# Kernel tuning notes

Measured on AMD Instinct MI355X. Metric: run time of the kernel, lower is better.

Reference implementation:

```python
import jax, jax.numpy as jnp
import numpy as np

CODEBOOK_SIZE = 1024
EMBED_DIM = 64
COMMITMENT_COST = 0.25


def setup_inputs() -> dict:
    key = jax.random.key(0)
    k1, k2 = jax.random.split(key)
    z = jax.random.normal(k1, (8, EMBED_DIM, 8192), dtype=jnp.float32)
    # torch init: uniform(-1/codebook_size, 1/codebook_size)
    codebook_weight = jax.random.uniform(
        k2, (CODEBOOK_SIZE, EMBED_DIM), dtype=jnp.float32,
        minval=-1.0 / CODEBOOK_SIZE, maxval=1.0 / CODEBOOK_SIZE)
    return {"z": z, "codebook_weight": codebook_weight}


def reference(z, codebook_weight):
    B, D, T = z.shape
    # [B*T, D]
    z_flat = jnp.transpose(z, (0, 2, 1)).reshape(-1, D)
    # squared euclidean distances to each code: ||z||^2 - 2 z.W^T + ||W||^2
    distances = (jnp.sum(z_flat * z_flat, axis=1, keepdims=True)
                 - 2.0 * z_flat @ codebook_weight.T
                 + jnp.sum(codebook_weight * codebook_weight, axis=1))
    codes = jnp.argmin(distances, axis=1)  # [B*T]
    z_q = codebook_weight[codes].reshape(B, T, D).transpose(0, 2, 1)  # [B, D, T]
    commitment_loss = jnp.mean((jax.lax.stop_gradient(z_q) - z) ** 2)
    codebook_loss = jnp.mean((z_q - jax.lax.stop_gradient(z)) ** 2)
    vq_loss = codebook_loss + COMMITMENT_COST * commitment_loss
    # straight-through estimator
    z_q_st = z + jax.lax.stop_gradient(z_q - z)
    return z_q_st, vq_loss, codes
```

## Files before the change

### kernel.cpp

```cpp
#include <hip/hip_runtime.h>


#define T_DIM 8192
#define D_DIM 64
#define C_DIM 1024
#define B_DIM 8
#define NROWS (B_DIM * T_DIM)
#define NELEM (B_DIM * D_DIM * T_DIM)
#define SEGS 4
#define CODES_PER_SEG (C_DIM / SEGS)
#define EPI_BLOCKS (NELEM / 4 / 256)

#define R64(M) M(0) M(1) M(2) M(3) M(4) M(5) M(6) M(7) \
  M(8) M(9) M(10) M(11) M(12) M(13) M(14) M(15) \
  M(16) M(17) M(18) M(19) M(20) M(21) M(22) M(23) \
  M(24) M(25) M(26) M(27) M(28) M(29) M(30) M(31) \
  M(32) M(33) M(34) M(35) M(36) M(37) M(38) M(39) \
  M(40) M(41) M(42) M(43) M(44) M(45) M(46) M(47) \
  M(48) M(49) M(50) M(51) M(52) M(53) M(54) M(55) \
  M(56) M(57) M(58) M(59) M(60) M(61) M(62) M(63)

#define SQ_(x) __fmul_rn(x, x)
#define AD_(a, b) __fadd_rn(a, b)

#define PAIRWISE64(p, dst) \
  float pr0 = SQ_(p##0);  pr0 = AD_(pr0, SQ_(p##8));  pr0 = AD_(pr0, SQ_(p##16)); pr0 = AD_(pr0, SQ_(p##24)); pr0 = AD_(pr0, SQ_(p##32)); pr0 = AD_(pr0, SQ_(p##40)); pr0 = AD_(pr0, SQ_(p##48)); pr0 = AD_(pr0, SQ_(p##56)); \
  float pr1 = SQ_(p##1);  pr1 = AD_(pr1, SQ_(p##9));  pr1 = AD_(pr1, SQ_(p##17)); pr1 = AD_(pr1, SQ_(p##25)); pr1 = AD_(pr1, SQ_(p##33)); pr1 = AD_(pr1, SQ_(p##41)); pr1 = AD_(pr1, SQ_(p##49)); pr1 = AD_(pr1, SQ_(p##57)); \
  float pr2 = SQ_(p##2);  pr2 = AD_(pr2, SQ_(p##10)); pr2 = AD_(pr2, SQ_(p##18)); pr2 = AD_(pr2, SQ_(p##26)); pr2 = AD_(pr2, SQ_(p##34)); pr2 = AD_(pr2, SQ_(p##42)); pr2 = AD_(pr2, SQ_(p##50)); pr2 = AD_(pr2, SQ_(p##58)); \
  float pr3 = SQ_(p##3);  pr3 = AD_(pr3, SQ_(p##11)); pr3 = AD_(pr3, SQ_(p##19)); pr3 = AD_(pr3, SQ_(p##27)); pr3 = AD_(pr3, SQ_(p##35)); pr3 = AD_(pr3, SQ_(p##43)); pr3 = AD_(pr3, SQ_(p##51)); pr3 = AD_(pr3, SQ_(p##59)); \
  float pr4 = SQ_(p##4);  pr4 = AD_(pr4, SQ_(p##12)); pr4 = AD_(pr4, SQ_(p##20)); pr4 = AD_(pr4, SQ_(p##28)); pr4 = AD_(pr4, SQ_(p##36)); pr4 = AD_(pr4, SQ_(p##44)); pr4 = AD_(pr4, SQ_(p##52)); pr4 = AD_(pr4, SQ_(p##60)); \
  float pr5 = SQ_(p##5);  pr5 = AD_(pr5, SQ_(p##13)); pr5 = AD_(pr5, SQ_(p##21)); pr5 = AD_(pr5, SQ_(p##29)); pr5 = AD_(pr5, SQ_(p##37)); pr5 = AD_(pr5, SQ_(p##45)); pr5 = AD_(pr5, SQ_(p##53)); pr5 = AD_(pr5, SQ_(p##61)); \
  float pr6 = SQ_(p##6);  pr6 = AD_(pr6, SQ_(p##14)); pr6 = AD_(pr6, SQ_(p##22)); pr6 = AD_(pr6, SQ_(p##30)); pr6 = AD_(pr6, SQ_(p##38)); pr6 = AD_(pr6, SQ_(p##46)); pr6 = AD_(pr6, SQ_(p##54)); pr6 = AD_(pr6, SQ_(p##62)); \
  float pr7 = SQ_(p##7);  pr7 = AD_(pr7, SQ_(p##15)); pr7 = AD_(pr7, SQ_(p##23)); pr7 = AD_(pr7, SQ_(p##31)); pr7 = AD_(pr7, SQ_(p##39)); pr7 = AD_(pr7, SQ_(p##47)); pr7 = AD_(pr7, SQ_(p##55)); pr7 = AD_(pr7, SQ_(p##63)); \
  float dst = AD_(AD_(AD_(pr0, pr1), AD_(pr2, pr3)), AD_(AD_(pr4, pr5), AD_(pr6, pr7)));

__global__ __launch_bounds__(256, 2)
void vq_dist_kernel(const float* __restrict__ z,
                    const float* __restrict__ cb,
                    float2* __restrict__ pairs) {
    const int tid = threadIdx.x;
    const int row = blockIdx.x * 256 + tid;
    const int seg = blockIdx.y;
    const int c0 = seg * CODES_PER_SEG;
    const int b = row >> 13;
    const int t = row & (T_DIM - 1);

    __shared__ float wsqs[CODES_PER_SEG];
    __shared__ float4 zl[16][256];

    {
        const float* wp = cb + ((size_t)(c0 + tid) << 6);
#define LOADW(k) float w##k = wp[k];
        R64(LOADW)
#undef LOADW
        PAIRWISE64(w, s)
        wsqs[tid] = s;
    }

    const float* zp = z + (size_t)b * (D_DIM * T_DIM) + t;
#define LOADZ(k) float z##k = zp[(size_t)k * T_DIM];
    R64(LOADZ)
#undef LOADZ
    PAIRWISE64(z, zsq)
    zl[ 0][tid] = make_float4(z0,  z1,  z2,  z3);
    zl[ 1][tid] = make_float4(z4,  z5,  z6,  z7);
    zl[ 2][tid] = make_float4(z8,  z9,  z10, z11);
    zl[ 3][tid] = make_float4(z12, z13, z14, z15);
    zl[ 4][tid] = make_float4(z16, z17, z18, z19);
    zl[ 5][tid] = make_float4(z20, z21, z22, z23);
    zl[ 6][tid] = make_float4(z24, z25, z26, z27);
    zl[ 7][tid] = make_float4(z28, z29, z30, z31);
    zl[ 8][tid] = make_float4(z32, z33, z34, z35);
    zl[ 9][tid] = make_float4(z36, z37, z38, z39);
    zl[10][tid] = make_float4(z40, z41, z42, z43);
    zl[11][tid] = make_float4(z44, z45, z46, z47);
    zl[12][tid] = make_float4(z48, z49, z50, z51);
    zl[13][tid] = make_float4(z52, z53, z54, z55);
    zl[14][tid] = make_float4(z56, z57, z58, z59);
    zl[15][tid] = make_float4(z60, z61, z62, z63);
    __syncthreads();

    float bestd = 3.4e38f;
    int besti = 0;
#pragma unroll 1
    for (int cc = 0; cc < CODES_PER_SEG; cc += 8) {
        const float* wp = cb + ((size_t)(c0 + cc) << 6);
        float a0 = 0.f, a1 = 0.f, a2 = 0.f, a3 = 0.f;
        float a4 = 0.f, a5 = 0.f, a6 = 0.f, a7 = 0.f;
#pragma unroll
        for (int kk = 0; kk < 16; ++kk) {
            const float4 zk = zl[kk][tid];
            const int k4 = kk << 2;
#define CHAIN(n) \
            a##n = fmaf(zk.x, wp[(n << 6) + k4 + 0], a##n); \
            a##n = fmaf(zk.y, wp[(n << 6) + k4 + 1], a##n); \
            a##n = fmaf(zk.z, wp[(n << 6) + k4 + 2], a##n); \
            a##n = fmaf(zk.w, wp[(n << 6) + k4 + 3], a##n);
            CHAIN(0) CHAIN(1) CHAIN(2) CHAIN(3)
            CHAIN(4) CHAIN(5) CHAIN(6) CHAIN(7)
#undef CHAIN
        }
        const float4 wqA = *(const float4*)(&wsqs[cc]);
        const float4 wqB = *(const float4*)(&wsqs[cc + 4]);
        float d0 = __fadd_rn(__fsub_rn(zsq, __fmul_rn(2.0f, a0)), wqA.x);
        float d1 = __fadd_rn(__fsub_rn(zsq, __fmul_rn(2.0f, a1)), wqA.y);
        float d2 = __fadd_rn(__fsub_rn(zsq, __fmul_rn(2.0f, a2)), wqA.z);
        float d3 = __fadd_rn(__fsub_rn(zsq, __fmul_rn(2.0f, a3)), wqA.w);
        float d4 = __fadd_rn(__fsub_rn(zsq, __fmul_rn(2.0f, a4)), wqB.x);
        float d5 = __fadd_rn(__fsub_rn(zsq, __fmul_rn(2.0f, a5)), wqB.y);
        float d6 = __fadd_rn(__fsub_rn(zsq, __fmul_rn(2.0f, a6)), wqB.z);
        float d7 = __fadd_rn(__fsub_rn(zsq, __fmul_rn(2.0f, a7)), wqB.w);
        if (d0 < bestd) { bestd = d0; besti = c0 + cc + 0; }
        if (d1 < bestd) { bestd = d1; besti = c0 + cc + 1; }
        if (d2 < bestd) { bestd = d2; besti = c0 + cc + 2; }
        if (d3 < bestd) { bestd = d3; besti = c0 + cc + 3; }
        if (d4 < bestd) { bestd = d4; besti = c0 + cc + 4; }
        if (d5 < bestd) { bestd = d5; besti = c0 + cc + 5; }
        if (d6 < bestd) { bestd = d6; besti = c0 + cc + 6; }
        if (d7 < bestd) { bestd = d7; besti = c0 + cc + 7; }
    }
    pairs[seg * NROWS + row] = make_float2(bestd, (float)besti);
}

__global__ void vq_argmin_kernel(const float2* __restrict__ pairs,
                                 float* __restrict__ codes) {
    int row = blockIdx.x * blockDim.x + threadIdx.x;
    float2 best = pairs[row];
#pragma unroll
    for (int s = 1; s < SEGS; ++s) {
        float2 p = pairs[s * NROWS + row];
        if (p.x < best.x) best = p;
    }
    codes[row] = best.y;
}

__global__ void vq_epilogue_kernel(const float* __restrict__ z,
                                   const float* __restrict__ cb,
                                   const float* __restrict__ codes,
                                   float* __restrict__ out,
                                   double* __restrict__ partials) {
    const int q = blockIdx.x * 256 + threadIdx.x;
    const int i = q << 2;
    const int t = i & (T_DIM - 1);
    const int bd = i >> 13;
    const int d = bd & (D_DIM - 1);
    const int b = bd >> 6;
    const int row = (b << 13) | t;

    float4 cr = *(const float4*)(codes + row);
    float4 zv = *(const float4*)(z + i);
    float w0 = cb[((int)cr.x << 6) + d];
    float w1 = cb[((int)cr.y << 6) + d];
    float w2 = cb[((int)cr.z << 6) + d];
    float w3 = cb[((int)cr.w << 6) + d];

    float4 df = make_float4(w0 - zv.x, w1 - zv.y, w2 - zv.z, w3 - zv.w);
    float4 o = make_float4(zv.x + df.x, zv.y + df.y, zv.z + df.z, zv.w + df.w);
    *(float4*)(out + i) = o;

    double v = (double)df.x * df.x + (double)df.y * df.y +
               (double)df.z * df.z + (double)df.w * df.w;
#pragma unroll
    for (int o2 = 32; o2 > 0; o2 >>= 1) v += __shfl_down(v, o2, 64);

    __shared__ double red[4];
    if ((threadIdx.x & 63) == 0) red[threadIdx.x >> 6] = v;
    __syncthreads();
    if (threadIdx.x == 0)
        partials[blockIdx.x] = ((red[0] + red[1]) + (red[2] + red[3]));
}

__global__ void vq_loss_kernel(const double* __restrict__ partials,
                               float* __restrict__ out_loss) {
    double s = 0.0;
    for (int i = threadIdx.x; i < EPI_BLOCKS; i += 256) s += partials[i];
#pragma unroll
    for (int o = 32; o > 0; o >>= 1) s += __shfl_down(s, o, 64);
    __shared__ double red[4];
    if ((threadIdx.x & 63) == 0) red[threadIdx.x >> 6] = s;
    __syncthreads();
    if (threadIdx.x == 0) {
        double tot = (red[0] + red[1]) + (red[2] + red[3]);
        out_loss[0] = (float)(1.25 * tot / (double)NELEM);
    }
}

extern "C" void kernel_launch(void* const* d_in, const int* in_sizes, int n_in,
                              void* d_out, int out_size, void* d_ws, size_t ws_size,
                              hipStream_t stream) {
    const float* z  = (const float*)d_in[0];
    const float* cb = (const float*)d_in[1];

    float* out      = (float*)d_out;
    float* out_loss = out + NELEM;
    float* codes    = out + NELEM + 1;

    char* ws    = (char*)d_ws;
    double* partials = (double*)(ws);
    float2* pairs = (float2*)(ws + 32768);

    dim3 grid1(NROWS / 256, SEGS);
    vq_dist_kernel<<<grid1, 256, 0, stream>>>(z, cb, pairs);

    vq_argmin_kernel<<<NROWS / 256, 256, 0, stream>>>(pairs, codes);

    vq_epilogue_kernel<<<EPI_BLOCKS, 256, 0, stream>>>(z, cb, codes, out, partials);

    vq_loss_kernel<<<1, 256, 0, stream>>>(partials, out_loss);
}
```

Measured before the change: 268.2 us.

## Hold codebook rows in registers and reduce argmin across wavefront lanes

The distance kernel is restructured so that each lane keeps two codebook rows in registers and loops over the 256 z rows staged in shared memory. The argmin is found with a wavefront shuffle-min and a ballot, then a cross-wave reduction through shared memory. Segments drop from 4 to 2, so each block covers 512 codes. This removes the per-thread scalar codebook loads from global/cache in the inner loop, but adds a 6-step shuffle reduction and ballots for every row and more register pressure from the 128 held floats. Tie-breaking should stay lowest index within a wave, and across waves and segments a strict less-than comparison keeps the earlier code.

```diff
diff --git a/kernel.cpp b/kernel.cpp
--- a/kernel.cpp
+++ b/kernel.cpp
@@ -7,8 +7,7 @@
 #define B_DIM 8
 #define NROWS (B_DIM * T_DIM)
 #define NELEM (B_DIM * D_DIM * T_DIM)
-#define SEGS 4
-#define CODES_PER_SEG (C_DIM / SEGS)
+#define SEGS 2
 #define EPI_BLOCKS (NELEM / 4 / 256)
 
 #define R64(M) M(0) M(1) M(2) M(3) M(4) M(5) M(6) M(7) \
@@ -34,92 +33,114 @@
   float pr7 = SQ_(p##7);  pr7 = AD_(pr7, SQ_(p##15)); pr7 = AD_(pr7, SQ_(p##23)); pr7 = AD_(pr7, SQ_(p##31)); pr7 = AD_(pr7, SQ_(p##39)); pr7 = AD_(pr7, SQ_(p##47)); pr7 = AD_(pr7, SQ_(p##55)); pr7 = AD_(pr7, SQ_(p##63)); \
   float dst = AD_(AD_(AD_(pr0, pr1), AD_(pr2, pr3)), AD_(AD_(pr4, pr5), AD_(pr6, pr7)));
 
+#define WSQ_OF(arr, dst) float dst; { \
+  float c0 = SQ_(arr[0].x); c0=AD_(c0,SQ_(arr[2].x)); c0=AD_(c0,SQ_(arr[4].x)); c0=AD_(c0,SQ_(arr[6].x)); c0=AD_(c0,SQ_(arr[8].x)); c0=AD_(c0,SQ_(arr[10].x)); c0=AD_(c0,SQ_(arr[12].x)); c0=AD_(c0,SQ_(arr[14].x)); \
+  float c1 = SQ_(arr[0].y); c1=AD_(c1,SQ_(arr[2].y)); c1=AD_(c1,SQ_(arr[4].y)); c1=AD_(c1,SQ_(arr[6].y)); c1=AD_(c1,SQ_(arr[8].y)); c1=AD_(c1,SQ_(arr[10].y)); c1=AD_(c1,SQ_(arr[12].y)); c1=AD_(c1,SQ_(arr[14].y)); \
+  float c2 = SQ_(arr[0].z); c2=AD_(c2,SQ_(arr[2].z)); c2=AD_(c2,SQ_(arr[4].z)); c2=AD_(c2,SQ_(arr[6].z)); c2=AD_(c2,SQ_(arr[8].z)); c2=AD_(c2,SQ_(arr[10].z)); c2=AD_(c2,SQ_(arr[12].z)); c2=AD_(c2,SQ_(arr[14].z)); \
+  float c3 = SQ_(arr[0].w); c3=AD_(c3,SQ_(arr[2].w)); c3=AD_(c3,SQ_(arr[4].w)); c3=AD_(c3,SQ_(arr[6].w)); c3=AD_(c3,SQ_(arr[8].w)); c3=AD_(c3,SQ_(arr[10].w)); c3=AD_(c3,SQ_(arr[12].w)); c3=AD_(c3,SQ_(arr[14].w)); \
+  float c4 = SQ_(arr[1].x); c4=AD_(c4,SQ_(arr[3].x)); c4=AD_(c4,SQ_(arr[5].x)); c4=AD_(c4,SQ_(arr[7].x)); c4=AD_(c4,SQ_(arr[9].x)); c4=AD_(c4,SQ_(arr[11].x)); c4=AD_(c4,SQ_(arr[13].x)); c4=AD_(c4,SQ_(arr[15].x)); \
+  float c5 = SQ_(arr[1].y); c5=AD_(c5,SQ_(arr[3].y)); c5=AD_(c5,SQ_(arr[5].y)); c5=AD_(c5,SQ_(arr[7].y)); c5=AD_(c5,SQ_(arr[9].y)); c5=AD_(c5,SQ_(arr[11].y)); c5=AD_(c5,SQ_(arr[13].y)); c5=AD_(c5,SQ_(arr[15].y)); \
+  float c6 = SQ_(arr[1].z); c6=AD_(c6,SQ_(arr[3].z)); c6=AD_(c6,SQ_(arr[5].z)); c6=AD_(c6,SQ_(arr[7].z)); c6=AD_(c6,SQ_(arr[9].z)); c6=AD_(c6,SQ_(arr[11].z)); c6=AD_(c6,SQ_(arr[13].z)); c6=AD_(c6,SQ_(arr[15].z)); \
+  float c7 = SQ_(arr[1].w); c7=AD_(c7,SQ_(arr[3].w)); c7=AD_(c7,SQ_(arr[5].w)); c7=AD_(c7,SQ_(arr[7].w)); c7=AD_(c7,SQ_(arr[9].w)); c7=AD_(c7,SQ_(arr[11].w)); c7=AD_(c7,SQ_(arr[13].w)); c7=AD_(c7,SQ_(arr[15].w)); \
+  dst = AD_(AD_(AD_(c0, c1), AD_(c2, c3)), AD_(AD_(c4, c5), AD_(c6, c7))); }
+
 __global__ __launch_bounds__(256, 2)
 void vq_dist_kernel(const float* __restrict__ z,
                     const float* __restrict__ cb,
                     float2* __restrict__ pairs) {
-    const int tid = threadIdx.x;
-    const int row = blockIdx.x * 256 + tid;
-    const int seg = blockIdx.y;
-    const int c0 = seg * CODES_PER_SEG;
-    const int b = row >> 13;
-    const int t = row & (T_DIM - 1);
-
-    __shared__ float wsqs[CODES_PER_SEG];
+    const int tid  = threadIdx.x;
+    const int wid  = tid >> 6;
+    const int lane = tid & 63;
+    const int seg  = blockIdx.y;
+    const int row0 = blockIdx.x * 256;
+    const int b    = row0 >> 13;
+    const int t0   = row0 & (T_DIM - 1);
+
     __shared__ float4 zl[16][256];
+    __shared__ float  zsql[256];
+    __shared__ float2 res[4][256];
 
     {
-        const float* wp = cb + ((size_t)(c0 + tid) << 6);
-#define LOADW(k) float w##k = wp[k];
-        R64(LOADW)
-#undef LOADW
-        PAIRWISE64(w, s)
-        wsqs[tid] = s;
-    }
-
-    const float* zp = z + (size_t)b * (D_DIM * T_DIM) + t;
+        const float* zp = z + (size_t)b * (D_DIM * T_DIM) + (t0 + tid);
 #define LOADZ(k) float z##k = zp[(size_t)k * T_DIM];
-    R64(LOADZ)
+        R64(LOADZ)
 #undef LOADZ
-    PAIRWISE64(z, zsq)
-    zl[ 0][tid] = make_float4(z0,  z1,  z2,  z3);
-    zl[ 1][tid] = make_float4(z4,  z5,  z6,  z7);
-    zl[ 2][tid] = make_float4(z8,  z9,  z10, z11);
-    zl[ 3][tid] = make_float4(z12, z13, z14, z15);
-    zl[ 4][tid] = make_float4(z16, z17, z18, z19);
-    zl[ 5][tid] = make_float4(z20, z21, z22, z23);
-    zl[ 6][tid] = make_float4(z24, z25, z26, z27);
-    zl[ 7][tid] = make_float4(z28, z29, z30, z31);
-    zl[ 8][tid] = make_float4(z32, z33, z34, z35);
-    zl[ 9][tid] = make_float4(z36, z37, z38, z39);
-    zl[10][tid] = make_float4(z40, z41, z42, z43);
-    zl[11][tid] = make_float4(z44, z45, z46, z47);
-    zl[12][tid] = make_float4(z48, z49, z50, z51);
-    zl[13][tid] = make_float4(z52, z53, z54, z55);
-    zl[14][tid] = make_float4(z56, z57, z58, z59);
-    zl[15][tid] = make_float4(z60, z61, z62, z63);
-    __syncthreads();
-
-    float bestd = 3.4e38f;
-    int besti = 0;
-#pragma unroll 1
-    for (int cc = 0; cc < CODES_PER_SEG; cc += 8) {
-        const float* wp = cb + ((size_t)(c0 + cc) << 6);
-        float a0 = 0.f, a1 = 0.f, a2 = 0.f, a3 = 0.f;
-        float a4 = 0.f, a5 = 0.f, a6 = 0.f, a7 = 0.f;
+        PAIRWISE64(z, zsq)
+        zsql[tid] = zsq;
+        zl[ 0][tid] = make_float4(z0,  z1,  z2,  z3);
+        zl[ 1][tid] = make_float4(z4,  z5,  z6,  z7);
+        zl[ 2][tid] = make_float4(z8,  z9,  z10, z11);
+        zl[ 3][tid] = make_float4(z12, z13, z14, z15);
+        zl[ 4][tid] = make_float4(z16, z17, z18, z19);
+        zl[ 5][tid] = make_float4(z20, z21, z22, z23);
+        zl[ 6][tid] = make_float4(z24, z25, z26, z27);
+        zl[ 7][tid] = make_float4(z28, z29, z30, z31);
+        zl[ 8][tid] = make_float4(z32, z33, z34, z35);
+        zl[ 9][tid] = make_float4(z36, z37, z38, z39);
+        zl[10][tid] = make_float4(z40, z41, z42, z43);
+        zl[11][tid] = make_float4(z44, z45, z46, z47);
+        zl[12][tid] = make_float4(z48, z49, z50, z51);
+        zl[13][tid] = make_float4(z52, z53, z54, z55);
+        zl[14][tid] = make_float4(z56, z57, z58, z59);
+        zl[15][tid] = make_float4(z60, z61, z62, z63);
+    }
+
+    const int cbase = seg * 512 + wid * 128;
+    const int cA = cbase + lane;
+    const int cB = cA + 64;
+    float4 wa[16], wb[16];
+    {
+        const float4* wpa = (const float4*)(cb + ((size_t)cA << 6));
+        const float4* wpb = (const float4*)(cb + ((size_t)cB << 6));
+#pragma unroll
+        for (int kk = 0; kk < 16; ++kk) { wa[kk] = wpa[kk]; wb[kk] = wpb[kk]; }
+    }
+    WSQ_OF(wa, wsqA)
+    WSQ_OF(wb, wsqB)
+    __syncthreads();
+
+#pragma unroll 2
+    for (int r = 0; r < 256; ++r) {
+        float a = 0.f, a2 = 0.f;
 #pragma unroll
         for (int kk = 0; kk < 16; ++kk) {
-            const float4 zk = zl[kk][tid];
-            const int k4 = kk << 2;
-#define CHAIN(n) \
-            a##n = fmaf(zk.x, wp[(n << 6) + k4 + 0], a##n); \
-            a##n = fmaf(zk.y, wp[(n << 6) + k4 + 1], a##n); \
-            a##n = fmaf(zk.z, wp[(n << 6) + k4 + 2], a##n); \
-            a##n = fmaf(zk.w, wp[(n << 6) + k4 + 3], a##n);
-            CHAIN(0) CHAIN(1) CHAIN(2) CHAIN(3)
-            CHAIN(4) CHAIN(5) CHAIN(6) CHAIN(7)
-#undef CHAIN
+            const float4 zc = zl[kk][r];
+            a  = fmaf(zc.x, wa[kk].x, a);
+            a  = fmaf(zc.y, wa[kk].y, a);
+            a  = fmaf(zc.z, wa[kk].z, a);
+            a  = fmaf(zc.w, wa[kk].w, a);
+            a2 = fmaf(zc.x, wb[kk].x, a2);
+            a2 = fmaf(zc.y, wb[kk].y, a2);
+            a2 = fmaf(zc.z, wb[kk].z, a2);
+            a2 = fmaf(zc.w, wb[kk].w, a2);
         }
-        const float4 wqA = *(const float4*)(&wsqs[cc]);
-        const float4 wqB = *(const float4*)(&wsqs[cc + 4]);
-        float d0 = __fadd_rn(__fsub_rn(zsq, __fmul_rn(2.0f, a0)), wqA.x);
-        float d1 = __fadd_rn(__fsub_rn(zsq, __fmul_rn(2.0f, a1)), wqA.y);
-        float d2 = __fadd_rn(__fsub_rn(zsq, __fmul_rn(2.0f, a2)), wqA.z);
-        float d3 = __fadd_rn(__fsub_rn(zsq, __fmul_rn(2.0f, a3)), wqA.w);
-        float d4 = __fadd_rn(__fsub_rn(zsq, __fmul_rn(2.0f, a4)), wqB.x);
-        float d5 = __fadd_rn(__fsub_rn(zsq, __fmul_rn(2.0f, a5)), wqB.y);
-        float d6 = __fadd_rn(__fsub_rn(zsq, __fmul_rn(2.0f, a6)), wqB.z);
-        float d7 = __fadd_rn(__fsub_rn(zsq, __fmul_rn(2.0f, a7)), wqB.w);
-        if (d0 < bestd) { bestd = d0; besti = c0 + cc + 0; }
-        if (d1 < bestd) { bestd = d1; besti = c0 + cc + 1; }
-        if (d2 < bestd) { bestd = d2; besti = c0 + cc + 2; }
-        if (d3 < bestd) { bestd = d3; besti = c0 + cc + 3; }
-        if (d4 < bestd) { bestd = d4; besti = c0 + cc + 4; }
-        if (d5 < bestd) { bestd = d5; besti = c0 + cc + 5; }
-        if (d6 < bestd) { bestd = d6; besti = c0 + cc + 6; }
-        if (d7 < bestd) { bestd = d7; besti = c0 + cc + 7; }
-    }
-    pairs[seg * NROWS + row] = make_float2(bestd, (float)besti);
+        const float zr = zsql[r];
+        const float dA = __fadd_rn(__fsub_rn(zr, __fmul_rn(2.0f, a)),  wsqA);
+        const float dB = __fadd_rn(__fsub_rn(zr, __fmul_rn(2.0f, a2)), wsqB);
+        const bool tookB = (dB < dA);
+        const float d = tookB ? dB : dA;
+        float m = d;
+#pragma unroll
+        for (int off = 32; off > 0; off >>= 1)
+            m = fminf(m, __shfl_xor(m, off, 64));
+        const unsigned long long mA = __ballot((!tookB) && (d == m));
+        const unsigned long long mB = __ballot(tookB && (d == m));
+        int code;
+        if (mA) code = cbase + (__ffsll((long long)mA) - 1);
+        else    code = cbase + 64 + (__ffsll((long long)mB) - 1);
+        if (lane == 0) res[wid][r] = make_float2(m, (float)code);
+    }
+    __syncthreads();
+
+    {
+        float2 best = res[0][tid];
+#pragma unroll
+        for (int w = 1; w < 4; ++w) {
+            const float2 p = res[w][tid];
+            if (p.x < best.x) best = p;
+        }
+        pairs[seg * NROWS + row0 + tid] = best;
+    }
 }
 
 __global__ void vq_argmin_kernel(const float2* __restrict__ pairs,
```

Result: slower. 275.9 us (+2.9%).
